# Optimization experiments

Measured on AMD Instinct MI355X. Metric: run time of the kernel, lower is better.

The kernel has to match this reference:

```python
import jax, jax.numpy as jnp
import numpy as np

B, Tu, Tm, Tz = 32, 128, 128, 32
V, H, E = 10000, 512, 128
S = E + H  # state_size


def setup_inputs() -> dict:
    key = jax.random.key(0)
    ks = jax.random.split(key, 24)
    u_input = jax.random.randint(ks[0], (B, Tu), 0, V)
    m_input = jax.random.randint(ks[1], (B, Tm), 0, V)
    pv_z_idx = jax.random.randint(ks[2], (B, Tz), 0, V)
    inp = {
        'u_input': u_input,
        'u_input_1hot': jax.nn.one_hot(u_input, V, dtype=jnp.float32),
        'u_hiddens': jax.random.normal(ks[3], (B, Tu, H), jnp.float32),
        'm_input': m_input,
        'm_input_1hot': jax.nn.one_hot(m_input, V, dtype=jnp.float32),
        'm_hiddens': jax.random.normal(ks[4], (B, Tm, H), jnp.float32),
        'pv_z_prob': jax.nn.softmax(jax.random.normal(ks[5], (B, Tz, V), jnp.float32), axis=-1),
        'pv_z_hidden': jax.random.normal(ks[6], (B, Tz, H), jnp.float32),
        'pv_z_idx': pv_z_idx,
        'emb_zt': jax.random.normal(ks[7], (B, 1, E), jnp.float32),
        'last_hidden': jax.random.normal(ks[8], (1, B, H), jnp.float32),
        # Attn params (concat attention: v . tanh(W [h; enc]))
        'W_attn': jax.random.normal(ks[9], (H, 2 * H), jnp.float32) * 0.02,
        'b_attn': jnp.zeros((H,), jnp.float32),
        'v_attn': jax.random.normal(ks[10], (H,), jnp.float32) * 0.05,
        # GRU params (torch gate order r,z,n)
        'W_ih': jax.random.normal(ks[11], (3 * H, S), jnp.float32) * 0.02,
        'W_hh': jax.random.normal(ks[12], (3 * H, H), jnp.float32) * 0.02,
        'b_ih': jnp.zeros((3 * H,), jnp.float32),
        'b_hh': jnp.zeros((3 * H,), jnp.float32),
        # generation / copy-score projections
        'W_gen': jax.random.normal(ks[13], (V, S), jnp.float32) * 0.02,
        'b_gen': jnp.zeros((V,), jnp.float32),
        'W_cpu': jax.random.normal(ks[14], (S, H), jnp.float32) * 0.02,
        'b_cpu': jnp.zeros((S,), jnp.float32),
        'W_cpm': jax.random.normal(ks[15], (S, H), jnp.float32) * 0.02,
        'b_cpm': jnp.zeros((S,), jnp.float32),
        'W_cppz': jax.random.normal(ks[16], (S, H), jnp.float32) * 0.02,
        'b_cppz': jnp.zeros((S,), jnp.float32),
    }
    return inp


def reference(u_input, u_input_1hot, u_hiddens, m_input, m_input_1hot, m_hiddens,
              pv_z_prob, pv_z_hidden, pv_z_idx, emb_zt, last_hidden,
              W_attn, b_attn, v_attn, W_ih, W_hh, b_ih, b_hh,
              W_gen, b_gen, W_cpu, b_cpu, W_cpm, b_cpm, W_cppz, b_cppz):
    Bv, Tuv, Vv = u_input_1hot.shape
    Tmv = m_hiddens.shape[1]
    t_input = emb_zt  # [B,1,E] (enable_selc_read=False)

    # ---- concat attention over [u; m; pv_z] hiddens ----
    enc = jnp.concatenate([u_hiddens, m_hiddens, pv_z_hidden], axis=1)  # [B,T,H]
    h0 = jnp.transpose(last_hidden, (1, 0, 2))  # [B,1,H]
    hid_rep = jnp.broadcast_to(h0, (Bv, enc.shape[1], h0.shape[2]))
    energy = jnp.tanh(jnp.einsum('bth,gh->btg', jnp.concatenate([hid_rep, enc], axis=2), W_attn) + b_attn)
    attn_w = jax.nn.softmax(jnp.einsum('bth,h->bt', energy, v_attn), axis=1)
    context = jnp.einsum('bt,bth->bh', attn_w, enc)[:, None, :]  # [B,1,H]

    # ---- single GRU step (torch gate order r,z,n) ----
    x = jnp.concatenate([t_input, context], axis=2)[:, 0, :]  # [B,E+H]
    h = h0[:, 0, :]
    gi = x @ W_ih.T + b_ih
    gh = h @ W_hh.T + b_hh
    i_r, i_z, i_n = jnp.split(gi, 3, axis=1)
    h_r, h_z, h_n = jnp.split(gh, 3, axis=1)
    r = jax.nn.sigmoid(i_r + h_r)
    z = jax.nn.sigmoid(i_z + h_z)
    n = jnp.tanh(i_n + r * h_n)
    h_new = (1.0 - z) * n + z * h  # [B,H]
    gru_out = h_new[:, None, :]
    last_hidden_new = h_new[None, :, :]

    # ---- generation + copy scores ----
    st = jnp.concatenate([h_new, t_input[:, 0, :]], axis=1)  # [B,E+H]
    score_g = st @ W_gen.T + b_gen  # [B,V]
    sc_u = jnp.einsum('bts,bs->bt', jnp.tanh(jnp.einsum('bth,sh->bts', u_hiddens, W_cpu) + b_cpu), st)
    sc_m = jnp.einsum('bts,bs->bt', jnp.tanh(jnp.einsum('bth,sh->bts', m_hiddens, W_cpm) + b_cpm), st)
    sc_pz = jnp.einsum('bts,bs->bt', jnp.tanh(jnp.einsum('bth,sh->bts', pv_z_hidden, W_cppz) + b_cppz), st)
    probs = jax.nn.softmax(jnp.concatenate([score_g, sc_u, sc_m, sc_pz], axis=1), axis=1)

    p_g = probs[:, :Vv]
    p_u = probs[:, Vv:Vv + Tuv]
    p_m = probs[:, Vv + Tuv:Vv + Tuv + Tmv]
    p_pz = probs[:, Vv + Tuv + Tmv:]
    prob_out = (p_g
                + jnp.einsum('bt,btv->bv', p_u, u_input_1hot)
                + jnp.einsum('bt,btv->bv', p_m, m_input_1hot)
                + jnp.einsum('bt,btv->bv', p_pz, pv_z_prob))
    return (prob_out, last_hidden_new, gru_out)
```

## Files before the change

### kernel.cpp

```cpp
#include <hip/hip_runtime.h>
#include <math.h>

#define B   32
#define TU  128
#define TM  128
#define TZ  32
#define TENC 288
#define V   10000
#define H   512
#define E   128
#define S   640
#define G3  1536
#define NLOG (V + TENC)

#define WS_Q      0
#define WS_SCORE  (WS_Q + B*H)
#define WS_CTX    (WS_SCORE + B*TENC)
#define WS_GI     (WS_CTX + B*H)
#define WS_GH     (WS_GI + B*G3)
#define WS_ST     (WS_GH + B*G3)
#define WS_LOGIT  (WS_ST + B*S)
#define WS_PCOPY  (WS_LOGIT + B*NLOG)
#define WS_F_TOTAL (WS_PCOPY + B*TENC)

#define BF_WA2  0
#define BF_WCP  (BF_WA2 + 512*512)
#define BF_ENC  (BF_WCP + 3*640*512)
#define BF_ST   (BF_ENC + B*TENC*H)
#define BF_TANH (BF_ST + B*S)

typedef __attribute__((ext_vector_type(8))) short bf16x8_t;
typedef __attribute__((ext_vector_type(4))) float f32x4_t;
typedef __attribute__((ext_vector_type(16))) float f32x16_t;

__device__ __forceinline__ float fast_tanh(float x) {
    return 1.f - 2.f / (__expf(2.f * x) + 1.f);
}

__device__ __forceinline__ unsigned short f2bf(float x) {
    unsigned int u = __float_as_uint(x);
    u += 0x7fffu + ((u >> 16) & 1u);
    return (unsigned short)(u >> 16);
}

__device__ __forceinline__ float bf2f(unsigned short u) {
    return __uint_as_float(((unsigned int)u) << 16);
}

__device__ __forceinline__ bf16x8_t cvt8(const float* p) {
    float4 a = *(const float4*)(p);
    float4 b = *(const float4*)(p + 4);
    bf16x8_t r;
    r[0] = (short)f2bf(a.x); r[1] = (short)f2bf(a.y);
    r[2] = (short)f2bf(a.z); r[3] = (short)f2bf(a.w);
    r[4] = (short)f2bf(b.x); r[5] = (short)f2bf(b.y);
    r[6] = (short)f2bf(b.z); r[7] = (short)f2bf(b.w);
    return r;
}

__device__ __forceinline__ const float* enc_row(const float* u, const float* m,
                                                const float* pz, int b, int t) {
    if (t < TU) return u + ((size_t)b * TU + t) * H;
    if (t < TU + TM) return m + ((size_t)b * TM + (t - TU)) * H;
    return pz + ((size_t)b * TZ + (t - TU - TM)) * H;
}

#define CVT_WA2_END  65536
#define CVT_TOTAL    (CVT_WA2_END + 3*81920)
#define CVTE_TOTAL   (B * TENC * 128)
#define CVT_ALL      (CVT_TOTAL + CVTE_TOTAL)
__global__ __launch_bounds__(256) void k_cvt_all(const float* __restrict__ W_attn,
                                                 const float* __restrict__ W_cpu,
                                                 const float* __restrict__ W_cpm,
                                                 const float* __restrict__ W_cppz,
                                                 const float* __restrict__ u_h,
                                                 const float* __restrict__ m_h,
                                                 const float* __restrict__ pz_h,
                                                 unsigned short* __restrict__ bf) {
    int idx = blockIdx.x * 256 + threadIdx.x;
    if (idx >= CVT_ALL) return;
    const float* src;
    unsigned short* dst;
    if (idx < CVT_WA2_END) {
        int g = idx >> 7, c4 = idx & 127;
        int k = c4 * 4, kt = k >> 5, kin = k & 31;
        src = W_attn + (size_t)g * 1024 + 512 + k;
        dst = bf + BF_WA2 + kt * (512 * 32) + g * 32 + kin;
    } else if (idx < CVT_TOTAL) {
        int r = idx - CVT_WA2_END;
        int seg = r / 81920, q = r % 81920;
        int s = q >> 7, c4 = q & 127;
        int k = c4 * 4, kt = k >> 5, kin = k & 31;
        const float* s0 = (seg == 0) ? W_cpu : (seg == 1) ? W_cpm : W_cppz;
        src = s0 + (size_t)s * 512 + k;
        dst = bf + BF_WCP + seg * 327680 + kt * (640 * 32) + s * 32 + kin;
    } else {
        int e = idx - CVT_TOTAL;
        int b = e / (TENC * 128);
        int r = e % (TENC * 128);
        int t = r >> 7, c4 = r & 127;
        int k = c4 * 4, kt = k >> 5, kin = k & 31;
        src = enc_row(u_h, m_h, pz_h, b, t) + k;
        dst = bf + BF_ENC + (((size_t)b * 16 + kt) * TENC + t) * 32 + kin;
    }
    float4 v = *(const float4*)src;
    ushort4 o;
    o.x = f2bf(v.x); o.y = f2bf(v.y); o.z = f2bf(v.z); o.w = f2bf(v.w);
    *(ushort4*)dst = o;
}

__global__ __launch_bounds__(256) void k_q_mfma(const float* __restrict__ last_h,
                                                const float* __restrict__ W_attn,
                                                const float* __restrict__ b_attn,
                                                float* __restrict__ ws) {
    int tid = threadIdx.x, wave = tid >> 6, lane = tid & 63;
    int m = lane & 31, khalf = lane >> 5;
    int n = blockIdx.x * 128 + wave * 32 + (lane & 31);
    const float* aptr = last_h + (size_t)m * H + khalf * 8;
    const float* bptr = W_attn + (size_t)n * 1024 + khalf * 8;
    f32x16_t acc = {};
    for (int k0 = 0; k0 < 512; k0 += 16) {
        bf16x8_t a = cvt8(aptr + k0);
        bf16x8_t bb = cvt8(bptr + k0);
        acc = __builtin_amdgcn_mfma_f32_32x32x16_bf16(a, bb, acc, 0, 0, 0);
    }
    float bg = b_attn[n];
#pragma unroll
    for (int r = 0; r < 16; ++r) {
        int row = (r & 3) + 8 * (r >> 2) + 4 * khalf;
        ws[WS_Q + row * H + n] = acc[r] + bg;
    }
}

__global__ __launch_bounds__(512) void k_enc_mfma(const unsigned short* __restrict__ bf,
                                                  const float* __restrict__ v_attn,
                                                  const float* __restrict__ b_cpu,
                                                  const float* __restrict__ b_cpm,
                                                  const float* __restrict__ b_cppz,
                                                  float* __restrict__ ws,
                                                  unsigned short* __restrict__ bft) {
    int blk = blockIdx.x;
    int b = blk / 9, t0 = (blk % 9) * 32;
    int tid = threadIdx.x, wave = tid >> 6, lane = tid & 63;
    int n16 = lane & 15, quad = lane >> 4;
    int seg = (t0 < TU) ? 0 : (t0 < TU + TM) ? 1 : 2;
    const float* bias = (seg == 0) ? b_cpu : (seg == 1) ? b_cpm : b_cppz;
    const unsigned short* abase =
        bf + BF_ENC + (((size_t)b * 16) * TENC + t0 + n16) * 32 + quad * 8;
    const unsigned short* wa =
        bf + BF_WA2 + (wave * 4) * (16 * 32) + n16 * 32 + quad * 8;
    const unsigned short* wc =
        bf + BF_WCP + seg * 327680 + (wave * 5) * (16 * 32) + n16 * 32 + quad * 8;
    f32x4_t accA[2][4], accC[2][5];
#pragma unroll
    for (int tl = 0; tl < 2; ++tl) {
#pragma unroll
        for (int j = 0; j < 4; ++j) accA[tl][j] = (f32x4_t){0.f, 0.f, 0.f, 0.f};
#pragma unroll
        for (int j = 0; j < 5; ++j) accC[tl][j] = (f32x4_t){0.f, 0.f, 0.f, 0.f};
    }
    for (int kt = 0; kt < 16; ++kt) {
        bf16x8_t a0 = *(const bf16x8_t*)(abase + (size_t)kt * TENC * 32);
        bf16x8_t a1 = *(const bf16x8_t*)(abase + (size_t)kt * TENC * 32 + 16 * 32);
        const unsigned short* wak = wa + (size_t)kt * 512 * 32;
        const unsigned short* wck = wc + (size_t)kt * 640 * 32;
#pragma unroll
        for (int j = 0; j < 4; ++j) {
            bf16x8_t bb = *(const bf16x8_t*)(wak + j * (16 * 32));
            accA[0][j] = __builtin_amdgcn_mfma_f32_16x16x32_bf16(a0, bb, accA[0][j], 0, 0, 0);
            accA[1][j] = __builtin_amdgcn_mfma_f32_16x16x32_bf16(a1, bb, accA[1][j], 0, 0, 0);
        }
#pragma unroll
        for (int j = 0; j < 5; ++j) {
            bf16x8_t bb = *(const bf16x8_t*)(wck + j * (16 * 32));
            accC[0][j] = __builtin_amdgcn_mfma_f32_16x16x32_bf16(a0, bb, accC[0][j], 0, 0, 0);
            accC[1][j] = __builtin_amdgcn_mfma_f32_16x16x32_bf16(a1, bb, accC[1][j], 0, 0, 0);
        }
    }
    float sval[2][4] = {{0.f, 0.f, 0.f, 0.f}, {0.f, 0.f, 0.f, 0.f}};
#pragma unroll
    for (int j = 0; j < 4; ++j) {
        int g = (wave * 4 + j) * 16 + n16;
        float q = ws[WS_Q + b * H + g];
        float va = v_attn[g];
#pragma unroll
        for (int tl = 0; tl < 2; ++tl)
#pragma unroll
            for (int r = 0; r < 4; ++r)
                sval[tl][r] += fast_tanh(accA[tl][j][r] + q) * va;
    }
#pragma unroll
    for (int tl = 0; tl < 2; ++tl)
#pragma unroll
        for (int r = 0; r < 4; ++r)
#pragma unroll
            for (int off = 8; off > 0; off >>= 1)
                sval[tl][r] += __shfl_down(sval[tl][r], off, 64);
    __shared__ float red[8][32];
    if (n16 == 0)
#pragma unroll
        for (int tl = 0; tl < 2; ++tl)
#pragma unroll
            for (int r = 0; r < 4; ++r)
                red[wave][tl * 16 + quad * 4 + r] = sval[tl][r];
#pragma unroll
    for (int j = 0; j < 5; ++j) {
        int s = (wave * 5 + j) * 16 + n16;
        float bi = bias[s];
#pragma unroll
        for (int tl = 0; tl < 2; ++tl)
#pragma unroll
            for (int r = 0; r < 4; ++r) {
                int t = t0 + tl * 16 + quad * 4 + r;
                bft[BF_TANH + ((size_t)b * TENC + t) * S + s] =
                    f2bf(fast_tanh(accC[tl][j][r] + bi));
            }
    }
    __syncthreads();
    if (tid < 32) {
        float v = 0.f;
#pragma unroll
        for (int w = 0; w < 8; ++w) v += red[w][tid];
        ws[WS_SCORE + b * TENC + t0 + tid] = v;
    }
}

__global__ __launch_bounds__(256) void k_softmax_ctx(const unsigned short* __restrict__ bf,
                                                     float* __restrict__ ws) {
    int b = blockIdx.x, tid = threadIdx.x;
    __shared__ float wsm[TENC];
    __shared__ float red1[4], red2[4];
    float local = -1e30f;
    for (int t = tid; t < TENC; t += 256) {
        float s = ws[WS_SCORE + b * TENC + t];
        wsm[t] = s;
        local = fmaxf(local, s);
    }
    int lane = tid & 63, wv = tid >> 6;
    for (int off = 32; off > 0; off >>= 1) local = fmaxf(local, __shfl_down(local, off, 64));
    if (lane == 0) red1[wv] = local;
    __syncthreads();
    float mx = fmaxf(fmaxf(red1[0], red1[1]), fmaxf(red1[2], red1[3]));
    float ls = 0.f;
    for (int t = tid; t < TENC; t += 256) {
        float e = __expf(wsm[t] - mx);
        wsm[t] = e;
        ls += e;
    }
    for (int off = 32; off > 0; off >>= 1) ls += __shfl_down(ls, off, 64);
    if (lane == 0) red2[wv] = ls;
    __syncthreads();
    float inv = 1.f / (red2[0] + red2[1] + red2[2] + red2[3]);

    int h = blockIdx.y * 256 + tid;
    int kt = h >> 5, hin = h & 31;
    const unsigned short* ep = bf + BF_ENC + ((size_t)b * 16 + kt) * TENC * 32 + hin;
    float a0 = 0.f, a1 = 0.f, a2 = 0.f, a3 = 0.f;
    for (int t = 0; t < TENC; t += 4) {
        a0 += wsm[t]     * bf2f(ep[(t)     * 32]);
        a1 += wsm[t + 1] * bf2f(ep[(t + 1) * 32]);
        a2 += wsm[t + 2] * bf2f(ep[(t + 2) * 32]);
        a3 += wsm[t + 3] * bf2f(ep[(t + 3) * 32]);
    }
    ws[WS_CTX + b * H + h] = (a0 + a1 + a2 + a3) * inv;
}

__global__ __launch_bounds__(256) void k_gru_mfma(const float* __restrict__ emb,
                                                  const float* __restrict__ last_h,
                                                  const float* __restrict__ W_ih,
                                                  const float* __restrict__ W_hh,
                                                  const float* __restrict__ b_ih,
                                                  const float* __restrict__ b_hh,
                                                  float* __restrict__ ws) {
    int tid = threadIdx.x, wave = tid >> 6, lane = tid & 63;
    int m = lane & 31, khalf = lane >> 5;
    int n = blockIdx.x * 128 + wave * 32 + (lane & 31);
    const float* bi_row = W_ih + (size_t)n * S + khalf * 8;
    f32x16_t acc_i = {};
    for (int k0 = 0; k0 < S; k0 += 16) {
        int ks = k0 + khalf * 8;
        const float* ap = (ks < E) ? (emb + m * E + ks)
                                   : (ws + WS_CTX + m * H + (ks - E));
        bf16x8_t a = cvt8(ap);
        bf16x8_t bb = cvt8(bi_row + k0);
        acc_i = __builtin_amdgcn_mfma_f32_32x32x16_bf16(a, bb, acc_i, 0, 0, 0);
    }
    const float* bh_row = W_hh + (size_t)n * H + khalf * 8;
    const float* ah = last_h + (size_t)m * H + khalf * 8;
    f32x16_t acc_h = {};
    for (int k0 = 0; k0 < H; k0 += 16) {
        bf16x8_t a = cvt8(ah + k0);
        bf16x8_t bb = cvt8(bh_row + k0);
        acc_h = __builtin_amdgcn_mfma_f32_32x32x16_bf16(a, bb, acc_h, 0, 0, 0);
    }
    float bi = b_ih[n], bh = b_hh[n];
#pragma unroll
    for (int r = 0; r < 16; ++r) {
        int row = (r & 3) + 8 * (r >> 2) + 4 * khalf;
        ws[WS_GI + row * G3 + n] = acc_i[r] + bi;
        ws[WS_GH + row * G3 + n] = acc_h[r] + bh;
    }
}

__global__ __launch_bounds__(256) void k_gru_combine(const float* __restrict__ emb,
                                                     const float* __restrict__ last_hidden,
                                                     float* __restrict__ ws,
                                                     unsigned short* __restrict__ bf,
                                                     float* __restrict__ out) {
    int i = blockIdx.x * 256 + threadIdx.x;
    int b = i >> 9, h = i & 511;
    float gi_r = ws[WS_GI + b * G3 + h];
    float gi_z = ws[WS_GI + b * G3 + H + h];
    float gi_n = ws[WS_GI + b * G3 + 2 * H + h];
    float gh_r = ws[WS_GH + b * G3 + h];
    float gh_z = ws[WS_GH + b * G3 + H + h];
    float gh_n = ws[WS_GH + b * G3 + 2 * H + h];
    float rr = 1.f / (1.f + __expf(-(gi_r + gh_r)));
    float zz = 1.f / (1.f + __expf(-(gi_z + gh_z)));
    float nn = fast_tanh(gi_n + rr * gh_n);
    float hp = last_hidden[b * H + h];
    float hn = (1.f - zz) * nn + zz * hp;
    out[V * B + b * H + h] = hn;
    out[V * B + B * H + b * H + h] = hn;
    ws[WS_ST + b * S + h] = hn;
    bf[BF_ST + b * S + h] = f2bf(hn);
    if (h < E) {
        float ev = emb[b * E + h];
        ws[WS_ST + b * S + H + h] = ev;
        bf[BF_ST + b * S + H + h] = f2bf(ev);
    }
}

__global__ __launch_bounds__(256) void k_copy_reduce(const unsigned short* __restrict__ bf,
                                                     float* __restrict__ ws) {
    int blk = blockIdx.x;
    int b = blk / 18, t0 = (blk % 18) * 16;
    int tid = threadIdx.x, wave = tid >> 6, lane = tid & 63;
    __shared__ float st_s[S];
    for (int i = tid; i < S; i += 256) st_s[i] = ws[WS_ST + b * S + i];
    __syncthreads();
#pragma unroll
    for (int tl = 0; tl < 4; ++tl) {
        int t = t0 + wave * 4 + tl;
        const unsigned short* row = bf + BF_TANH + ((size_t)b * TENC + t) * S;
        float acc = 0.f;
#pragma unroll
        for (int i = 0; i < 10; ++i) {
            int s = lane + 64 * i;
            acc += bf2f(row[s]) * st_s[s];
        }
        for (int off = 32; off > 0; off >>= 1) acc += __shfl_down(acc, off, 64);
        if (lane == 0) ws[WS_LOGIT + (size_t)b * NLOG + V + t] = acc;
    }
}

__global__ __launch_bounds__(256) void k_score_g_mfma(const unsigned short* __restrict__ bf,
                                                      const float* __restrict__ W_gen,
                                                      const float* __restrict__ b_gen,
                                                      float* __restrict__ ws) {
    int tid = threadIdx.x, wave = tid >> 6, lane = tid & 63;
    int m = lane & 31, khalf = lane >> 5;
    int n = blockIdx.x * 128 + wave * 32 + (lane & 31);
    int nr = (n < V) ? n : (V - 1);
    const unsigned short* aptr = bf + BF_ST + (size_t)m * S + khalf * 8;
    const float* bptr = W_gen + (size_t)nr * S + khalf * 8;
    f32x16_t acc = {};
    for (int k0 = 0; k0 < S; k0 += 16) {
        bf16x8_t a = *(const bf16x8_t*)(aptr + k0);
        bf16x8_t bb = cvt8(bptr + k0);
        acc = __builtin_amdgcn_mfma_f32_32x32x16_bf16(a, bb, acc, 0, 0, 0);
    }
    if (n >= V) return;
    float bg = b_gen[n];
#pragma unroll
    for (int r = 0; r < 16; ++r) {
        int row = (r & 3) + 8 * (r >> 2) + 4 * khalf;
        ws[WS_LOGIT + (size_t)row * NLOG + n] = acc[r] + bg;
    }
}

__global__ __launch_bounds__(256) void k_softmax_scatter(const int* __restrict__ u_in,
                                                         const int* __restrict__ m_in,
                                                         float* __restrict__ ws,
                                                         float* __restrict__ out) {
    int b = blockIdx.x, tid = threadIdx.x;
    __shared__ float red1[4], red2[4];
    __shared__ float pcopy[TENC];
    const float* lg = ws + WS_LOGIT + (size_t)b * NLOG;
    float mx = -1e30f;
    for (int i = tid; i < NLOG; i += 256) mx = fmaxf(mx, lg[i]);
    int lane = tid & 63, wv = tid >> 6;
    for (int off = 32; off > 0; off >>= 1) mx = fmaxf(mx, __shfl_down(mx, off, 64));
    if (lane == 0) red1[wv] = mx;
    __syncthreads();
    mx = fmaxf(fmaxf(red1[0], red1[1]), fmaxf(red1[2], red1[3]));
    float sm = 0.f;
    for (int i = tid; i < NLOG; i += 256) sm += __expf(lg[i] - mx);
    for (int off = 32; off > 0; off >>= 1) sm += __shfl_down(sm, off, 64);
    if (lane == 0) red2[wv] = sm;
    __syncthreads();
    float inv = 1.f / (red2[0] + red2[1] + red2[2] + red2[3]);
    for (int i = tid; i < NLOG; i += 256) {
        float p = __expf(lg[i] - mx) * inv;
        if (i < V) out[b * V + i] = p;
        else pcopy[i - V] = p;
    }
    __syncthreads();
    if (tid < TU + TM) {
        int idx = (tid < TU) ? u_in[b * TU + tid] : m_in[b * TM + (tid - TU)];
        atomicAdd(&out[(size_t)b * V + idx], pcopy[tid]);
    } else if (tid < TENC) {
        ws[WS_PCOPY + b * TENC + tid] = pcopy[tid];
    }
}

__global__ __launch_bounds__(256) void k_pv(const float* __restrict__ pvp,
                                            const float* __restrict__ ws,
                                            float* __restrict__ out) {
    int b = blockIdx.y;
    int v = blockIdx.x * 256 + threadIdx.x;
    __shared__ float p[TZ];
    if (threadIdx.x < TZ) p[threadIdx.x] = ws[WS_PCOPY + b * TENC + TU + TM + threadIdx.x];
    __syncthreads();
    if (v >= V) return;
    float acc = 0.f;
#pragma unroll 4
    for (int t = 0; t < TZ; ++t) acc += p[t] * pvp[((size_t)b * TZ + t) * V + v];
    out[(size_t)b * V + v] += acc;
}

extern "C" void kernel_launch(void* const* d_in, const int* in_sizes, int n_in,
                              void* d_out, int out_size, void* d_ws, size_t ws_size,
                              hipStream_t stream) {
    const int*   u_input   = (const int*)d_in[0];
    const float* u_h       = (const float*)d_in[2];
    const int*   m_input   = (const int*)d_in[3];
    const float* m_h       = (const float*)d_in[5];
    const float* pv_prob   = (const float*)d_in[6];
    const float* pz_h      = (const float*)d_in[7];
    const float* emb       = (const float*)d_in[9];
    const float* last_h    = (const float*)d_in[10];
    const float* W_attn    = (const float*)d_in[11];
    const float* b_attn    = (const float*)d_in[12];
    const float* v_attn    = (const float*)d_in[13];
    const float* W_ih      = (const float*)d_in[14];
    const float* W_hh      = (const float*)d_in[15];
    const float* b_ih      = (const float*)d_in[16];
    const float* b_hh      = (const float*)d_in[17];
    const float* W_gen     = (const float*)d_in[18];
    const float* b_gen     = (const float*)d_in[19];
    const float* W_cpu     = (const float*)d_in[20];
    const float* b_cpu     = (const float*)d_in[21];
    const float* W_cpm     = (const float*)d_in[22];
    const float* b_cpm     = (const float*)d_in[23];
    const float* W_cppz    = (const float*)d_in[24];
    const float* b_cppz    = (const float*)d_in[25];
    float* ws  = (float*)d_ws;
    unsigned short* bf = (unsigned short*)(ws + WS_F_TOTAL);
    float* out = (float*)d_out;

    hipLaunchKernelGGL(k_cvt_all, dim3((CVT_ALL + 255) / 256), dim3(256), 0, stream,
                       W_attn, W_cpu, W_cpm, W_cppz, u_h, m_h, pz_h, bf);
    hipLaunchKernelGGL(k_q_mfma, dim3(4), dim3(256), 0, stream, last_h, W_attn, b_attn, ws);
    hipLaunchKernelGGL(k_enc_mfma, dim3(B * 9), dim3(512), 0, stream,
                       bf, v_attn, b_cpu, b_cpm, b_cppz, ws, bf);
    hipLaunchKernelGGL(k_softmax_ctx, dim3(B, 2), dim3(256), 0, stream, bf, ws);
    hipLaunchKernelGGL(k_gru_mfma, dim3(12), dim3(256), 0, stream,
                       emb, last_h, W_ih, W_hh, b_ih, b_hh, ws);
    hipLaunchKernelGGL(k_gru_combine, dim3(64), dim3(256), 0, stream, emb, last_h, ws, bf, out);
    hipLaunchKernelGGL(k_copy_reduce, dim3(B * 18), dim3(256), 0, stream, bf, ws);
    hipLaunchKernelGGL(k_score_g_mfma, dim3((V + 127) / 128), dim3(256), 0, stream,
                       bf, W_gen, b_gen, ws);
    hipLaunchKernelGGL(k_softmax_scatter, dim3(B), dim3(256), 0, stream,
                       u_input, m_input, ws, out);
    hipLaunchKernelGGL(k_pv, dim3(40, B), dim3(256), 0, stream, pv_prob, ws, out);
}
```

Before: 532.4 us.

## Fuse GRU combine into copy reduce, split GRU GEMMs, retune launch shapes

Merges the GRU gate-combine kernel into the copy-score reduction kernel. Each block recomputes h_new for its batch row in shared memory, and only the first block per row writes the outputs. The GRU input and hidden GEMMs become separate single-wave blocks, and the q and score_g MFMA kernels switch to 64-thread blocks with more blocks so more CUs are used. The context kernel handles two hidden columns per thread in one block per batch row. The final softmax caches the exponentials in shared memory instead of re-reading and recomputing them. The fusion saves one launch but makes 18 blocks per batch row recompute the same GRU combine.

```diff
diff --git a/kernel.cpp b/kernel.cpp
--- a/kernel.cpp
+++ b/kernel.cpp
@@ -109,13 +109,13 @@
     *(ushort4*)dst = o;
 }
 
-__global__ __launch_bounds__(256) void k_q_mfma(const float* __restrict__ last_h,
-                                                const float* __restrict__ W_attn,
-                                                const float* __restrict__ b_attn,
-                                                float* __restrict__ ws) {
-    int tid = threadIdx.x, wave = tid >> 6, lane = tid & 63;
+__global__ __launch_bounds__(64) void k_q_mfma(const float* __restrict__ last_h,
+                                               const float* __restrict__ W_attn,
+                                               const float* __restrict__ b_attn,
+                                               float* __restrict__ ws) {
+    int lane = threadIdx.x & 63;
     int m = lane & 31, khalf = lane >> 5;
-    int n = blockIdx.x * 128 + wave * 32 + (lane & 31);
+    int n = blockIdx.x * 32 + m;
     const float* aptr = last_h + (size_t)m * H + khalf * 8;
     const float* bptr = W_attn + (size_t)n * 1024 + khalf * 8;
     f32x16_t acc = {};
@@ -252,97 +252,109 @@
     __syncthreads();
     float inv = 1.f / (red2[0] + red2[1] + red2[2] + red2[3]);
 
-    int h = blockIdx.y * 256 + tid;
-    int kt = h >> 5, hin = h & 31;
+    int h2 = tid * 2;
+    int kt = h2 >> 5, hin = h2 & 31;
     const unsigned short* ep = bf + BF_ENC + ((size_t)b * 16 + kt) * TENC * 32 + hin;
-    float a0 = 0.f, a1 = 0.f, a2 = 0.f, a3 = 0.f;
-    for (int t = 0; t < TENC; t += 4) {
-        a0 += wsm[t]     * bf2f(ep[(t)     * 32]);
-        a1 += wsm[t + 1] * bf2f(ep[(t + 1) * 32]);
-        a2 += wsm[t + 2] * bf2f(ep[(t + 2) * 32]);
-        a3 += wsm[t + 3] * bf2f(ep[(t + 3) * 32]);
-    }
-    ws[WS_CTX + b * H + h] = (a0 + a1 + a2 + a3) * inv;
-}
-
-__global__ __launch_bounds__(256) void k_gru_mfma(const float* __restrict__ emb,
-                                                  const float* __restrict__ last_h,
-                                                  const float* __restrict__ W_ih,
-                                                  const float* __restrict__ W_hh,
-                                                  const float* __restrict__ b_ih,
-                                                  const float* __restrict__ b_hh,
-                                                  float* __restrict__ ws) {
-    int tid = threadIdx.x, wave = tid >> 6, lane = tid & 63;
+    float a00 = 0.f, a01 = 0.f, a10 = 0.f, a11 = 0.f;
+#pragma unroll 2
+    for (int t = 0; t < TENC; t += 2) {
+        ushort2 v0 = *(const ushort2*)(ep + (size_t)t * 32);
+        ushort2 v1 = *(const ushort2*)(ep + (size_t)(t + 1) * 32);
+        float w0 = wsm[t], w1 = wsm[t + 1];
+        a00 += w0 * bf2f(v0.x); a10 += w0 * bf2f(v0.y);
+        a01 += w1 * bf2f(v1.x); a11 += w1 * bf2f(v1.y);
+    }
+    ws[WS_CTX + b * H + h2]     = (a00 + a01) * inv;
+    ws[WS_CTX + b * H + h2 + 1] = (a10 + a11) * inv;
+}
+
+__global__ __launch_bounds__(64) void k_gru_mfma(const float* __restrict__ emb,
+                                                 const float* __restrict__ last_h,
+                                                 const float* __restrict__ W_ih,
+                                                 const float* __restrict__ W_hh,
+                                                 const float* __restrict__ b_ih,
+                                                 const float* __restrict__ b_hh,
+                                                 float* __restrict__ ws) {
+    int blk = blockIdx.x;
+    int lane = threadIdx.x & 63;
     int m = lane & 31, khalf = lane >> 5;
-    int n = blockIdx.x * 128 + wave * 32 + (lane & 31);
-    const float* bi_row = W_ih + (size_t)n * S + khalf * 8;
-    f32x16_t acc_i = {};
-    for (int k0 = 0; k0 < S; k0 += 16) {
-        int ks = k0 + khalf * 8;
-        const float* ap = (ks < E) ? (emb + m * E + ks)
-                                   : (ws + WS_CTX + m * H + (ks - E));
-        bf16x8_t a = cvt8(ap);
-        bf16x8_t bb = cvt8(bi_row + k0);
-        acc_i = __builtin_amdgcn_mfma_f32_32x32x16_bf16(a, bb, acc_i, 0, 0, 0);
-    }
-    const float* bh_row = W_hh + (size_t)n * H + khalf * 8;
-    const float* ah = last_h + (size_t)m * H + khalf * 8;
-    f32x16_t acc_h = {};
-    for (int k0 = 0; k0 < H; k0 += 16) {
-        bf16x8_t a = cvt8(ah + k0);
-        bf16x8_t bb = cvt8(bh_row + k0);
-        acc_h = __builtin_amdgcn_mfma_f32_32x32x16_bf16(a, bb, acc_h, 0, 0, 0);
-    }
-    float bi = b_ih[n], bh = b_hh[n];
-#pragma unroll
-    for (int r = 0; r < 16; ++r) {
-        int row = (r & 3) + 8 * (r >> 2) + 4 * khalf;
-        ws[WS_GI + row * G3 + n] = acc_i[r] + bi;
-        ws[WS_GH + row * G3 + n] = acc_h[r] + bh;
-    }
-}
-
-__global__ __launch_bounds__(256) void k_gru_combine(const float* __restrict__ emb,
-                                                     const float* __restrict__ last_hidden,
-                                                     float* __restrict__ ws,
-                                                     unsigned short* __restrict__ bf,
-                                                     float* __restrict__ out) {
-    int i = blockIdx.x * 256 + threadIdx.x;
-    int b = i >> 9, h = i & 511;
-    float gi_r = ws[WS_GI + b * G3 + h];
-    float gi_z = ws[WS_GI + b * G3 + H + h];
-    float gi_n = ws[WS_GI + b * G3 + 2 * H + h];
-    float gh_r = ws[WS_GH + b * G3 + h];
-    float gh_z = ws[WS_GH + b * G3 + H + h];
-    float gh_n = ws[WS_GH + b * G3 + 2 * H + h];
-    float rr = 1.f / (1.f + __expf(-(gi_r + gh_r)));
-    float zz = 1.f / (1.f + __expf(-(gi_z + gh_z)));
-    float nn = fast_tanh(gi_n + rr * gh_n);
-    float hp = last_hidden[b * H + h];
-    float hn = (1.f - zz) * nn + zz * hp;
-    out[V * B + b * H + h] = hn;
-    out[V * B + B * H + b * H + h] = hn;
-    ws[WS_ST + b * S + h] = hn;
-    bf[BF_ST + b * S + h] = f2bf(hn);
-    if (h < E) {
-        float ev = emb[b * E + h];
-        ws[WS_ST + b * S + H + h] = ev;
-        bf[BF_ST + b * S + H + h] = f2bf(ev);
-    }
-}
-
-__global__ __launch_bounds__(256) void k_copy_reduce(const unsigned short* __restrict__ bf,
-                                                     float* __restrict__ ws) {
+    if (blk < 48) {
+        int n = blk * 32 + m;
+        const float* bi_row = W_ih + (size_t)n * S + khalf * 8;
+        f32x16_t acc = {};
+        for (int k0 = 0; k0 < S; k0 += 16) {
+            int ks = k0 + khalf * 8;
+            const float* ap = (ks < E) ? (emb + m * E + ks)
+                                       : (ws + WS_CTX + m * H + (ks - E));
+            bf16x8_t a = cvt8(ap);
+            bf16x8_t bb = cvt8(bi_row + k0);
+            acc = __builtin_amdgcn_mfma_f32_32x32x16_bf16(a, bb, acc, 0, 0, 0);
+        }
+        float bi = b_ih[n];
+#pragma unroll
+        for (int r = 0; r < 16; ++r) {
+            int row = (r & 3) + 8 * (r >> 2) + 4 * khalf;
+            ws[WS_GI + row * G3 + n] = acc[r] + bi;
+        }
+    } else {
+        int n = (blk - 48) * 32 + m;
+        const float* bh_row = W_hh + (size_t)n * H + khalf * 8;
+        const float* ah = last_h + (size_t)m * H + khalf * 8;
+        f32x16_t acc = {};
+        for (int k0 = 0; k0 < H; k0 += 16) {
+            bf16x8_t a = cvt8(ah + k0);
+            bf16x8_t bb = cvt8(bh_row + k0);
+            acc = __builtin_amdgcn_mfma_f32_32x32x16_bf16(a, bb, acc, 0, 0, 0);
+        }
+        float bh = b_hh[n];
+#pragma unroll
+        for (int r = 0; r < 16; ++r) {
+            int row = (r & 3) + 8 * (r >> 2) + 4 * khalf;
+            ws[WS_GH + row * G3 + n] = acc[r] + bh;
+        }
+    }
+}
+
+__global__ __launch_bounds__(256) void k_fuse_copy(const float* __restrict__ emb,
+                                                   const float* __restrict__ last_hidden,
+                                                   const unsigned short* __restrict__ bft,
+                                                   float* __restrict__ ws,
+                                                   unsigned short* __restrict__ bf,
+                                                   float* __restrict__ out) {
     int blk = blockIdx.x;
     int b = blk / 18, t0 = (blk % 18) * 16;
-    int tid = threadIdx.x, wave = tid >> 6, lane = tid & 63;
+    int tid = threadIdx.x;
     __shared__ float st_s[S];
-    for (int i = tid; i < S; i += 256) st_s[i] = ws[WS_ST + b * S + i];
-    __syncthreads();
+    for (int h = tid; h < H; h += 256) {
+        float gi_r = ws[WS_GI + b * G3 + h];
+        float gi_z = ws[WS_GI + b * G3 + H + h];
+        float gi_n = ws[WS_GI + b * G3 + 2 * H + h];
+        float gh_r = ws[WS_GH + b * G3 + h];
+        float gh_z = ws[WS_GH + b * G3 + H + h];
+        float gh_n = ws[WS_GH + b * G3 + 2 * H + h];
+        float rr = 1.f / (1.f + __expf(-(gi_r + gh_r)));
+        float zz = 1.f / (1.f + __expf(-(gi_z + gh_z)));
+        float nn = fast_tanh(gi_n + rr * gh_n);
+        float hp = last_hidden[b * H + h];
+        float hn = (1.f - zz) * nn + zz * hp;
+        st_s[h] = hn;
+        if (t0 == 0) {
+            out[V * B + b * H + h] = hn;
+            out[V * B + B * H + b * H + h] = hn;
+            bf[BF_ST + b * S + h] = f2bf(hn);
+        }
+    }
+    if (tid < E) {
+        float ev = emb[b * E + tid];
+        st_s[H + tid] = ev;
+        if (t0 == 0) bf[BF_ST + b * S + H + tid] = f2bf(ev);
+    }
+    __syncthreads();
+    int wave = tid >> 6, lane = tid & 63;
 #pragma unroll
     for (int tl = 0; tl < 4; ++tl) {
         int t = t0 + wave * 4 + tl;
-        const unsigned short* row = bf + BF_TANH + ((size_t)b * TENC + t) * S;
+        const unsigned short* row = bft + BF_TANH + ((size_t)b * TENC + t) * S;
         float acc = 0.f;
 #pragma unroll
         for (int i = 0; i < 10; ++i) {
@@ -354,13 +366,13 @@
     }
 }
 
-__global__ __launch_bounds__(256) void k_score_g_mfma(const unsigned short* __restrict__ bf,
-                                                      const float* __restrict__ W_gen,
-                                                      const float* __restrict__ b_gen,
-                                                      float* __restrict__ ws) {
-    int tid = threadIdx.x, wave = tid >> 6, lane = tid & 63;
+__global__ __launch_bounds__(64) void k_score_g_mfma(const unsigned short* __restrict__ bf,
+                                                     const float* __restrict__ W_gen,
+                                                     const float* __restrict__ b_gen,
+                                                     float* __restrict__ ws) {
+    int lane = threadIdx.x & 63;
     int m = lane & 31, khalf = lane >> 5;
-    int n = blockIdx.x * 128 + wave * 32 + (lane & 31);
+    int n = blockIdx.x * 32 + m;
     int nr = (n < V) ? n : (V - 1);
     const unsigned short* aptr = bf + BF_ST + (size_t)m * S + khalf * 8;
     const float* bptr = W_gen + (size_t)nr * S + khalf * 8;
@@ -379,38 +391,47 @@
     }
 }
 
-__global__ __launch_bounds__(256) void k_softmax_scatter(const int* __restrict__ u_in,
+__global__ __launch_bounds__(512) void k_softmax_scatter(const int* __restrict__ u_in,
                                                          const int* __restrict__ m_in,
                                                          float* __restrict__ ws,
                                                          float* __restrict__ out) {
     int b = blockIdx.x, tid = threadIdx.x;
-    __shared__ float red1[4], red2[4];
-    __shared__ float pcopy[TENC];
+    __shared__ float red1[8], red2[8];
+    __shared__ float ex[NLOG];
     const float* lg = ws + WS_LOGIT + (size_t)b * NLOG;
     float mx = -1e30f;
-    for (int i = tid; i < NLOG; i += 256) mx = fmaxf(mx, lg[i]);
+    for (int i = tid; i < NLOG; i += 512) {
+        float v = lg[i];
+        ex[i] = v;
+        mx = fmaxf(mx, v);
+    }
     int lane = tid & 63, wv = tid >> 6;
     for (int off = 32; off > 0; off >>= 1) mx = fmaxf(mx, __shfl_down(mx, off, 64));
     if (lane == 0) red1[wv] = mx;
     __syncthreads();
-    mx = fmaxf(fmaxf(red1[0], red1[1]), fmaxf(red1[2], red1[3]));
+    mx = red1[0];
+#pragma unroll
+    for (int w = 1; w < 8; ++w) mx = fmaxf(mx, red1[w]);
     float sm = 0.f;
-    for (int i = tid; i < NLOG; i += 256) sm += __expf(lg[i] - mx);
+    for (int i = tid; i < NLOG; i += 512) {
+        float e = __expf(ex[i] - mx);
+        ex[i] = e;
+        sm += e;
+    }
     for (int off = 32; off > 0; off >>= 1) sm += __shfl_down(sm, off, 64);
     if (lane == 0) red2[wv] = sm;
     __syncthreads();
-    float inv = 1.f / (red2[0] + red2[1] + red2[2] + red2[3]);
-    for (int i = tid; i < NLOG; i += 256) {
-        float p = __expf(lg[i] - mx) * inv;
-        if (i < V) out[b * V + i] = p;
-        else pcopy[i - V] = p;
-    }
+    sm = red2[0];
+#pragma unroll
+    for (int w = 1; w < 8; ++w) sm += red2[w];
+    float inv = 1.f / sm;
+    for (int i = tid; i < V; i += 512) out[b * V + i] = ex[i] * inv;
     __syncthreads();
     if (tid < TU + TM) {
         int idx = (tid < TU) ? u_in[b * TU + tid] : m_in[b * TM + (tid - TU)];
-        atomicAdd(&out[(size_t)b * V + idx], pcopy[tid]);
+        atomicAdd(&out[(size_t)b * V + idx], ex[V + tid] * inv);
     } else if (tid < TENC) {
-        ws[WS_PCOPY + b * TENC + tid] = pcopy[tid];
+        ws[WS_PCOPY + b * TENC + tid] = ex[V + tid] * inv;
     }
 }
 
@@ -461,17 +482,17 @@
 
     hipLaunchKernelGGL(k_cvt_all, dim3((CVT_ALL + 255) / 256), dim3(256), 0, stream,
                        W_attn, W_cpu, W_cpm, W_cppz, u_h, m_h, pz_h, bf);
-    hipLaunchKernelGGL(k_q_mfma, dim3(4), dim3(256), 0, stream, last_h, W_attn, b_attn, ws);
+    hipLaunchKernelGGL(k_q_mfma, dim3(16), dim3(64), 0, stream, last_h, W_attn, b_attn, ws);
     hipLaunchKernelGGL(k_enc_mfma, dim3(B * 9), dim3(512), 0, stream,
                        bf, v_attn, b_cpu, b_cpm, b_cppz, ws, bf);
-    hipLaunchKernelGGL(k_softmax_ctx, dim3(B, 2), dim3(256), 0, stream, bf, ws);
-    hipLaunchKernelGGL(k_gru_mfma, dim3(12), dim3(256), 0, stream,
+    hipLaunchKernelGGL(k_softmax_ctx, dim3(B), dim3(256), 0, stream, bf, ws);
+    hipLaunchKernelGGL(k_gru_mfma, dim3(96), dim3(64), 0, stream,
                        emb, last_h, W_ih, W_hh, b_ih, b_hh, ws);
-    hipLaunchKernelGGL(k_gru_combine, dim3(64), dim3(256), 0, stream, emb, last_h, ws, bf, out);
-    hipLaunchKernelGGL(k_copy_reduce, dim3(B * 18), dim3(256), 0, stream, bf, ws);
-    hipLaunchKernelGGL(k_score_g_mfma, dim3((V + 127) / 128), dim3(256), 0, stream,
+    hipLaunchKernelGGL(k_fuse_copy, dim3(B * 18), dim3(256), 0, stream,
+                       emb, last_h, bf, ws, bf, out);
+    hipLaunchKernelGGL(k_score_g_mfma, dim3((V + 31) / 32), dim3(64), 0, stream,
                        bf, W_gen, b_gen, ws);
-    hipLaunchKernelGGL(k_softmax_scatter, dim3(B), dim3(256), 0, stream,
+    hipLaunchKernelGGL(k_softmax_scatter, dim3(B), dim3(512), 0, stream,
                        u_input, m_input, ws, out);
     hipLaunchKernelGGL(k_pv, dim3(40, B), dim3(256), 0, stream, pv_prob, ws, out);
 }
```

Result: faster. 500.7 us (-6.0%).
